# Optimization experiments

Measured on AMD Instinct MI355X. Metric: run time of the kernel, lower is better.

## Reference

```python
import jax, jax.numpy as jnp
import numpy as np

B, I, E, X, T, W = 32768, 512, 8, 128, 2, 64


def setup_inputs() -> dict:
    key = jax.random.key(0)
    ks = jax.random.split(key, 6)
    sc = lambda k, shape, s: (jax.random.normal(k, shape, jnp.float32) * s)
    return {
        "x": jax.random.normal(ks[0], (B, I), jnp.float32),
        "We": sc(ks[1], (E, I, X), 0.04),       # per-expert SLP weights
        "be": jnp.zeros((E, X), jnp.float32),
        "gates": sc(ks[2], (T, I, E), 0.04),    # per-task gating matrices (no softmax in original)
        "tW1": sc(ks[3], (T, X, W), 0.08),      # tower MLP layer 1
        "tb1": jnp.zeros((T, W), jnp.float32),
        "tW2": sc(ks[4], (T, W, 1), 0.1),       # tower MLP layer 2 (scalar head)
        "tb2": jnp.zeros((T, 1), jnp.float32),
    }


def reference(x, We, be, gates, tW1, tb1, tW2, tb2):
    # task gates: [T, B, E] (raw matmul, faithful to original: no softmax applied)
    g = jnp.einsum('bi,tie->tbe', x, gates)
    # expert SLPs (Linear + ReLU): [E, B, X]
    ex = jax.nn.relu(jnp.einsum('bi,eix->ebx', x, We) + be[:, None, :])
    # fused replacement of the nested expert_size x num_experts loop:
    # shared_info[t, b, i] = sum_j g[t,b,j] * ex[j,b,i]
    shared = jnp.einsum('tbe,ebx->tbx', g, ex)
    # tower MLPs: Linear -> ReLU -> Linear(1)
    h = jax.nn.relu(jnp.einsum('tbx,txw->tbw', shared, tW1) + tb1[:, None, :])
    out = jnp.einsum('tbw,two->tbo', h, tW2) + tb2[:, None, :]
    return out  # [T, B, 1], row t = task t's output
```

## Files before the change

kernel.cpp:

```cpp
#include <hip/hip_runtime.h>
#include <cstdint>
#include <cstddef>

#define NB 32768
#define KI 512
#define NE 8
#define NX 128
#define NT 2
#define NWD 64
#define BM 128
#define THREADS 512
#define SMEM_BYTES 163840
#define W2_BYTES (NE * KI * NX * 2)

typedef __attribute__((ext_vector_type(8))) short bf16x8;
typedef __attribute__((ext_vector_type(4))) float f32x4;

__device__ __forceinline__ unsigned short f2bf(float f) {
  union { float f; unsigned u; } v; v.f = f;
  return (unsigned short)((v.u + 0x7fffu + ((v.u >> 16) & 1u)) >> 16);
}

#define AS1(p) ((const __attribute__((address_space(1))) void*)(uintptr_t)(p))
#define AS3(p) ((__attribute__((address_space(3))) void*)(uintptr_t)(p))

__global__ __launch_bounds__(256) void repack_we_kernel(const float* __restrict__ We,
                                                        unsigned short* __restrict__ W2) {
  int tid = blockIdx.x * 256 + threadIdx.x;
  int col  = tid & (NX - 1);
  int kblk = (tid >> 7) & 63;
  int e    = tid >> 13;
  const float* src = We + ((size_t)e * KI + (size_t)kblk * 8) * NX + col;
  bf16x8 v;
#pragma unroll
  for (int j = 0; j < 8; ++j) v[j] = (short)f2bf(src[(size_t)j * NX]);
  *(bf16x8*)(W2 + (size_t)tid * 8) = v;
}

template <bool USE_WS>
__global__ __launch_bounds__(THREADS, 2)
void moe_fused_kernel(const float* __restrict__ x, const float* __restrict__ We,
                      const float* __restrict__ be, const float* __restrict__ gates,
                      const float* __restrict__ tW1, const float* __restrict__ tb1,
                      const float* __restrict__ tW2, const float* __restrict__ tb2,
                      const unsigned short* __restrict__ W2, float* __restrict__ out) {
  extern __shared__ char smem[];
  char* wbuf = smem + 131072;

  const int tid  = threadIdx.x;
  const int lane = tid & 63;
  const int wid  = tid >> 6;
  const int l15  = lane & 15;
  const int lhi  = lane >> 4;
  const int row0 = blockIdx.x * BM;

  f32x4 acc[8];
  f32x4 shacc[NT][8];
  f32x4 gacc = {0.f, 0.f, 0.f, 0.f};
#pragma unroll
  for (int t = 0; t < NT; ++t)
#pragma unroll
    for (int cf = 0; cf < 8; ++cf) shacc[t][cf] = (f32x4){0.f, 0.f, 0.f, 0.f};

  const int arow = wid * 16 + l15;
  const int asw  = (arow & 7) << 4;
  char* abase = smem + arow * 1024;

  auto stage_x = [&](int kk) {
    const int xr = tid >> 2;
    const int xs = tid & 3;
    const float* src = x + (size_t)(row0 + xr) * KI + kk * 64 + xs * 16;
    float4 a0 = ((const float4*)src)[0];
    float4 a1 = ((const float4*)src)[1];
    float4 a2 = ((const float4*)src)[2];
    float4 a3 = ((const float4*)src)[3];
    bf16x8 v0, v1;
    v0[0]=(short)f2bf(a0.x); v0[1]=(short)f2bf(a0.y); v0[2]=(short)f2bf(a0.z); v0[3]=(short)f2bf(a0.w);
    v0[4]=(short)f2bf(a1.x); v0[5]=(short)f2bf(a1.y); v0[6]=(short)f2bf(a1.z); v0[7]=(short)f2bf(a1.w);
    v1[0]=(short)f2bf(a2.x); v1[1]=(short)f2bf(a2.y); v1[2]=(short)f2bf(a2.z); v1[3]=(short)f2bf(a2.w);
    v1[4]=(short)f2bf(a3.x); v1[5]=(short)f2bf(a3.y); v1[6]=(short)f2bf(a3.z); v1[7]=(short)f2bf(a3.w);
    const int sw = (xr & 7) << 4;
    const int kb = kk * 128 + xs * 32;
    *(bf16x8*)(smem + xr * 1024 + ((kb) ^ sw)) = v0;
    *(bf16x8*)(smem + xr * 1024 + ((kb + 16) ^ sw)) = v1;
  };

  auto stage_w = [&](int e, int kk, int b) {
    if constexpr (USE_WS) {
      const char* gbase = (const char*)W2 + ((size_t)(e * 64 + kk * 8) * NX) * 16;
      char* lbase = wbuf + b * 16384 + wid * 1024;
      __builtin_amdgcn_global_load_lds(AS1(gbase + (wid * 64 + lane) * 16), AS3(lbase), 16, 0, 0);
      __builtin_amdgcn_global_load_lds(AS1(gbase + 8192 + (wid * 64 + lane) * 16), AS3(lbase + 8192), 16, 0, 0);
    } else {
      const int col = tid & 127;
      const int kb0 = tid >> 7;
#pragma unroll
      for (int h = 0; h < 2; ++h) {
        const int kblk = kb0 + h * 4;
        const float* src = We + ((size_t)e * KI + (size_t)(kk * 64 + kblk * 8)) * NX + col;
        bf16x8 v;
#pragma unroll
        for (int j = 0; j < 8; ++j) v[j] = (short)f2bf(src[(size_t)j * NX]);
        *(bf16x8*)(wbuf + b * 16384 + (kblk * NX + col) * 16) = v;
      }
    }
  };

  auto compute_chunk = [&](int kk, int b) {
#pragma unroll
    for (int ks = 0; ks < 2; ++ks) {
      bf16x8 a = *(const bf16x8*)(abase + ((kk * 128 + ks * 64 + lhi * 16) ^ asw));
      const char* bbase = wbuf + b * 16384 + ((ks * 4 + lhi) * NX + l15) * 16;
#pragma unroll
      for (int cf = 0; cf < 8; ++cf) {
        bf16x8 bfr = *(const bf16x8*)(bbase + cf * 256);
        acc[cf] = __builtin_amdgcn_mfma_f32_16x16x32_bf16(a, bfr, acc[cf], 0, 0, 0);
      }
    }
  };

  auto compute_g = [&]() {
    const int ct = l15 >> 3;
    const int ce = l15 & 7;
#pragma unroll
    for (int ks = 0; ks < 16; ++ks) {
      bf16x8 a = *(const bf16x8*)(abase + ((ks * 64 + lhi * 16) ^ asw));
      const float* gsrc = gates + (size_t)ct * (KI * NE) + (size_t)(ks * 32 + lhi * 8) * NE + ce;
      bf16x8 bv;
#pragma unroll
      for (int j = 0; j < 8; ++j) bv[j] = (short)f2bf(gsrc[j * NE]);
      gacc = __builtin_amdgcn_mfma_f32_16x16x32_bf16(a, bv, gacc, 0, 0, 0);
    }
  };

  auto epilogue = [&](int e) {
    float gv[NT][4];
#pragma unroll
    for (int t = 0; t < NT; ++t)
#pragma unroll
      for (int r = 0; r < 4; ++r)
        gv[t][r] = __shfl(gacc[r], (lane & 48) | (t * 8 + e), 64);
#pragma unroll
    for (int cf = 0; cf < 8; ++cf) {
      const float bev = be[e * NX + cf * 16 + l15];
#pragma unroll
      for (int r = 0; r < 4; ++r) {
        float ex = acc[cf][r] + bev;
        ex = fmaxf(ex, 0.f);
        shacc[0][cf][r] += gv[0][r] * ex;
        shacc[1][cf][r] += gv[1][r] * ex;
      }
    }
  };

  for (int e = 0; e < NE; ++e) {
#pragma unroll
    for (int cf = 0; cf < 8; ++cf) acc[cf] = (f32x4){0.f, 0.f, 0.f, 0.f};
    if (e == 0) stage_x(0);
    stage_w(e, 0, 0);
    __syncthreads();
    for (int kk = 0; kk < 8; ++kk) {
      if (kk < 7) {
        if (e == 0) stage_x(kk + 1);
        stage_w(e, kk + 1, (kk + 1) & 1);
      }
      compute_chunk(kk, kk & 1);
      __syncthreads();
    }
    if (e == 0) compute_g();
    epilogue(e);
  }

#pragma unroll
  for (int t = 0; t < NT; ++t)
#pragma unroll
    for (int cf = 0; cf < 8; ++cf)
#pragma unroll
      for (int r = 0; r < 4; ++r) {
        const int rr = wid * 16 + lhi * 4 + r;
        const int cc = cf * 16 + l15;
        *(unsigned short*)(smem + t * 32768 + rr * 256 + ((cc * 2) ^ ((rr & 7) << 4))) =
            f2bf(shacc[t][cf][r]);
      }
  __syncthreads();

#pragma unroll
  for (int t = 0; t < NT; ++t) {
    f32x4 hacc[4];
#pragma unroll
    for (int cf = 0; cf < 4; ++cf) hacc[cf] = (f32x4){0.f, 0.f, 0.f, 0.f};
    const int trow = wid * 16 + l15;
    const char* tbase = smem + t * 32768 + trow * 256;
    const int tsw = (trow & 7) << 4;
#pragma unroll
    for (int ks = 0; ks < 4; ++ks) {
      bf16x8 a = *(const bf16x8*)(tbase + ((ks * 64 + lhi * 16) ^ tsw));
#pragma unroll
      for (int cf = 0; cf < 4; ++cf) {
        const int col = cf * 16 + l15;
        const float* wsrc = tW1 + (size_t)t * (NX * NWD) + (size_t)(ks * 32 + lhi * 8) * NWD + col;
        bf16x8 bv;
#pragma unroll
        for (int j = 0; j < 8; ++j) bv[j] = (short)f2bf(wsrc[j * NWD]);
        hacc[cf] = __builtin_amdgcn_mfma_f32_16x16x32_bf16(a, bv, hacc[cf], 0, 0, 0);
      }
    }
    float p[4] = {0.f, 0.f, 0.f, 0.f};
#pragma unroll
    for (int cf = 0; cf < 4; ++cf) {
      const int col = cf * 16 + l15;
      const float b1 = tb1[t * NWD + col];
      const float w2 = tW2[t * NWD + col];
#pragma unroll
      for (int r = 0; r < 4; ++r) {
        float h = fmaxf(hacc[cf][r] + b1, 0.f);
        p[r] += h * w2;
      }
    }
#pragma unroll
    for (int r = 0; r < 4; ++r) {
      p[r] += __shfl_xor(p[r], 1, 64);
      p[r] += __shfl_xor(p[r], 2, 64);
      p[r] += __shfl_xor(p[r], 4, 64);
      p[r] += __shfl_xor(p[r], 8, 64);
    }
    if (l15 == 0) {
      const float b2 = tb2[t];
#pragma unroll
      for (int r = 0; r < 4; ++r)
        out[(size_t)t * NB + row0 + wid * 16 + lhi * 4 + r] = p[r] + b2;
    }
  }
}

extern "C" void kernel_launch(void* const* d_in, const int* in_sizes, int n_in,
                              void* d_out, int out_size, void* d_ws, size_t ws_size,
                              hipStream_t stream) {
  const float* x     = (const float*)d_in[0];
  const float* We    = (const float*)d_in[1];
  const float* be    = (const float*)d_in[2];
  const float* gates = (const float*)d_in[3];
  const float* tW1   = (const float*)d_in[4];
  const float* tb1   = (const float*)d_in[5];
  const float* tW2   = (const float*)d_in[6];
  const float* tb2   = (const float*)d_in[7];
  float* out = (float*)d_out;

  const bool use_ws = (d_ws != nullptr) && (ws_size >= (size_t)W2_BYTES);
  const int nblk = NB / BM;

  if (use_ws) {
    unsigned short* W2 = (unsigned short*)d_ws;
    hipFuncSetAttribute(reinterpret_cast<const void*>(moe_fused_kernel<true>),
                        hipFuncAttributeMaxDynamicSharedMemorySize, SMEM_BYTES);
    repack_we_kernel<<<(NE * KI * NX / 8) / 256, 256, 0, stream>>>(We, W2);
    moe_fused_kernel<true><<<nblk, THREADS, SMEM_BYTES, stream>>>(
        x, We, be, gates, tW1, tb1, tW2, tb2, W2, out);
  } else {
    hipFuncSetAttribute(reinterpret_cast<const void*>(moe_fused_kernel<false>),
                        hipFuncAttributeMaxDynamicSharedMemorySize, SMEM_BYTES);
    moe_fused_kernel<false><<<nblk, THREADS, SMEM_BYTES, stream>>>(
        x, We, be, gates, tW1, tb1, tW2, tb2, nullptr, out);
  }
}
```

Measured before the change: 66.69 us.

## Load expert weights directly from global into registers, shrink tile to 64 rows

```diff
diff --git a/kernel.cpp b/kernel.cpp
--- a/kernel.cpp
+++ b/kernel.cpp
@@ -8,10 +8,16 @@
 #define NX 128
 #define NT 2
 #define NWD 64
-#define BM 128
-#define THREADS 512
-#define SMEM_BYTES 163840
-#define W2_BYTES (NE * KI * NX * 2)
+#define BM 64
+#define THREADS 256
+#define SMEM_BYTES 65536
+
+#define W2_ELEMS (NE * KI * NX)
+#define G2_OFF   W2_ELEMS
+#define G2_ELEMS (64 * 16 * 8)
+#define T2_OFF   (G2_OFF + G2_ELEMS)
+#define T2_ELEMS (NT * 16 * 64 * 8)
+#define WS_NEED  ((size_t)(W2_ELEMS + G2_ELEMS + T2_ELEMS) * 2)
 
 typedef __attribute__((ext_vector_type(8))) short bf16x8;
 typedef __attribute__((ext_vector_type(4))) float f32x4;
@@ -21,11 +27,8 @@
   return (unsigned short)((v.u + 0x7fffu + ((v.u >> 16) & 1u)) >> 16);
 }
 
-#define AS1(p) ((const __attribute__((address_space(1))) void*)(uintptr_t)(p))
-#define AS3(p) ((__attribute__((address_space(3))) void*)(uintptr_t)(p))
-
 __global__ __launch_bounds__(256) void repack_we_kernel(const float* __restrict__ We,
-                                                        unsigned short* __restrict__ W2) {
+                                                        unsigned short* __restrict__ ws) {
   int tid = blockIdx.x * 256 + threadIdx.x;
   int col  = tid & (NX - 1);
   int kblk = (tid >> 7) & 63;
@@ -34,7 +37,34 @@
   bf16x8 v;
 #pragma unroll
   for (int j = 0; j < 8; ++j) v[j] = (short)f2bf(src[(size_t)j * NX]);
-  *(bf16x8*)(W2 + (size_t)tid * 8) = v;
+  *(bf16x8*)(ws + (size_t)tid * 8) = v;
+}
+
+__global__ __launch_bounds__(256) void repack_aux_kernel(const float* __restrict__ gates,
+                                                         const float* __restrict__ tW1,
+                                                         unsigned short* __restrict__ ws) {
+  int tid = threadIdx.x;
+#pragma unroll
+  for (int i = 0; i < 4; ++i) {
+    int f = i * 256 + tid;
+    int kb = f >> 4, col = f & 15;
+    int t = col >> 3, e = col & 7;
+    const float* src = gates + (size_t)t * (KI * NE) + (size_t)(kb * 8) * NE + e;
+    bf16x8 v;
+#pragma unroll
+    for (int j = 0; j < 8; ++j) v[j] = (short)f2bf(src[(size_t)j * NE]);
+    *(bf16x8*)(ws + G2_OFF + (size_t)f * 8) = v;
+  }
+#pragma unroll
+  for (int i = 0; i < 8; ++i) {
+    int f = i * 256 + tid;
+    int t = f >> 10, kb = (f >> 6) & 15, col = f & 63;
+    const float* src = tW1 + (size_t)t * (NX * NWD) + (size_t)(kb * 8) * NWD + col;
+    bf16x8 v;
+#pragma unroll
+    for (int j = 0; j < 8; ++j) v[j] = (short)f2bf(src[(size_t)j * NWD]);
+    *(bf16x8*)(ws + T2_OFF + (size_t)f * 8) = v;
+  }
 }
 
 template <bool USE_WS>
@@ -43,179 +73,198 @@
                       const float* __restrict__ be, const float* __restrict__ gates,
                       const float* __restrict__ tW1, const float* __restrict__ tb1,
                       const float* __restrict__ tW2, const float* __restrict__ tb2,
-                      const unsigned short* __restrict__ W2, float* __restrict__ out) {
+                      const unsigned short* __restrict__ ws, float* __restrict__ out) {
   extern __shared__ char smem[];
-  char* wbuf = smem + 131072;
-
   const int tid  = threadIdx.x;
   const int lane = tid & 63;
   const int wid  = tid >> 6;
   const int l15  = lane & 15;
   const int lhi  = lane >> 4;
+  const int wr   = wid >> 1;
+  const int wc   = wid & 1;
   const int row0 = blockIdx.x * BM;
 
-  f32x4 acc[8];
-  f32x4 shacc[NT][8];
-  f32x4 gacc = {0.f, 0.f, 0.f, 0.f};
+  {
+    const float4* xs4 = (const float4*)(x + (size_t)row0 * KI);
+#pragma unroll
+    for (int c = 0; c < 16; ++c) {
+      int i = c * 256 + tid;
+      float4 a0 = xs4[(size_t)i * 2];
+      float4 a1 = xs4[(size_t)i * 2 + 1];
+      bf16x8 v;
+      v[0] = (short)f2bf(a0.x); v[1] = (short)f2bf(a0.y);
+      v[2] = (short)f2bf(a0.z); v[3] = (short)f2bf(a0.w);
+      v[4] = (short)f2bf(a1.x); v[5] = (short)f2bf(a1.y);
+      v[6] = (short)f2bf(a1.z); v[7] = (short)f2bf(a1.w);
+      int row = i >> 6;
+      int kb  = (i & 63) * 16;
+      *(bf16x8*)(smem + row * 1024 + (kb ^ ((row & 7) << 4))) = v;
+    }
+  }
+  __syncthreads();
+
+  auto loadBfrag = [&](int e, int kblk, int cf) -> bf16x8 {
+    if constexpr (USE_WS) {
+      return *(const bf16x8*)(ws + ((size_t)(e * 64 + kblk) * NX + wc * 64 + cf * 16 + l15) * 8);
+    } else {
+      const float* src = We + ((size_t)e * KI + (size_t)kblk * 8) * NX + wc * 64 + cf * 16 + l15;
+      bf16x8 v;
+#pragma unroll
+      for (int j = 0; j < 8; ++j) v[j] = (short)f2bf(src[(size_t)j * NX]);
+      return v;
+    }
+  };
+  auto loadGfrag = [&](int kb) -> bf16x8 {
+    if constexpr (USE_WS) {
+      return *(const bf16x8*)(ws + G2_OFF + ((size_t)kb * 16 + l15) * 8);
+    } else {
+      int t = l15 >> 3, e = l15 & 7;
+      const float* src = gates + (size_t)t * (KI * NE) + (size_t)(kb * 8) * NE + e;
+      bf16x8 v;
+#pragma unroll
+      for (int j = 0; j < 8; ++j) v[j] = (short)f2bf(src[(size_t)j * NE]);
+      return v;
+    }
+  };
+  auto loadTfrag = [&](int t, int kb, int cf) -> bf16x8 {
+    if constexpr (USE_WS) {
+      return *(const bf16x8*)(ws + T2_OFF + ((size_t)(t * 16 + kb) * 64 + cf * 16 + l15) * 8);
+    } else {
+      const float* src = tW1 + (size_t)t * (NX * NWD) + (size_t)(kb * 8) * NWD + cf * 16 + l15;
+      bf16x8 v;
+#pragma unroll
+      for (int j = 0; j < 8; ++j) v[j] = (short)f2bf(src[(size_t)j * NWD]);
+      return v;
+    }
+  };
+
+  const int arow = wr * 32 + l15;
+  char* ab0 = smem + arow * 1024;
+  char* ab1 = smem + (arow + 16) * 1024;
+  const int asw = (arow & 7) << 4;
+  auto loadA = [&](int kk, int ks, int rf) -> bf16x8 {
+    int byte = (kk * 128 + ks * 64 + lhi * 16) ^ asw;
+    return *(const bf16x8*)((rf ? ab1 : ab0) + byte);
+  };
+
+  f32x4 acc[2][4];
+  f32x4 shacc[NT][2][4];
+  f32x4 gacc[2];
 #pragma unroll
   for (int t = 0; t < NT; ++t)
 #pragma unroll
-    for (int cf = 0; cf < 8; ++cf) shacc[t][cf] = (f32x4){0.f, 0.f, 0.f, 0.f};
-
-  const int arow = wid * 16 + l15;
-  const int asw  = (arow & 7) << 4;
-  char* abase = smem + arow * 1024;
-
-  auto stage_x = [&](int kk) {
-    const int xr = tid >> 2;
-    const int xs = tid & 3;
-    const float* src = x + (size_t)(row0 + xr) * KI + kk * 64 + xs * 16;
-    float4 a0 = ((const float4*)src)[0];
-    float4 a1 = ((const float4*)src)[1];
-    float4 a2 = ((const float4*)src)[2];
-    float4 a3 = ((const float4*)src)[3];
-    bf16x8 v0, v1;
-    v0[0]=(short)f2bf(a0.x); v0[1]=(short)f2bf(a0.y); v0[2]=(short)f2bf(a0.z); v0[3]=(short)f2bf(a0.w);
-    v0[4]=(short)f2bf(a1.x); v0[5]=(short)f2bf(a1.y); v0[6]=(short)f2bf(a1.z); v0[7]=(short)f2bf(a1.w);
-    v1[0]=(short)f2bf(a2.x); v1[1]=(short)f2bf(a2.y); v1[2]=(short)f2bf(a2.z); v1[3]=(short)f2bf(a2.w);
-    v1[4]=(short)f2bf(a3.x); v1[5]=(short)f2bf(a3.y); v1[6]=(short)f2bf(a3.z); v1[7]=(short)f2bf(a3.w);
-    const int sw = (xr & 7) << 4;
-    const int kb = kk * 128 + xs * 32;
-    *(bf16x8*)(smem + xr * 1024 + ((kb) ^ sw)) = v0;
-    *(bf16x8*)(smem + xr * 1024 + ((kb + 16) ^ sw)) = v1;
-  };
-
-  auto stage_w = [&](int e, int kk, int b) {
-    if constexpr (USE_WS) {
-      const char* gbase = (const char*)W2 + ((size_t)(e * 64 + kk * 8) * NX) * 16;
-      char* lbase = wbuf + b * 16384 + wid * 1024;
-      __builtin_amdgcn_global_load_lds(AS1(gbase + (wid * 64 + lane) * 16), AS3(lbase), 16, 0, 0);
-      __builtin_amdgcn_global_load_lds(AS1(gbase + 8192 + (wid * 64 + lane) * 16), AS3(lbase + 8192), 16, 0, 0);
-    } else {
-      const int col = tid & 127;
-      const int kb0 = tid >> 7;
-#pragma unroll
-      for (int h = 0; h < 2; ++h) {
-        const int kblk = kb0 + h * 4;
-        const float* src = We + ((size_t)e * KI + (size_t)(kk * 64 + kblk * 8)) * NX + col;
-        bf16x8 v;
-#pragma unroll
-        for (int j = 0; j < 8; ++j) v[j] = (short)f2bf(src[(size_t)j * NX]);
-        *(bf16x8*)(wbuf + b * 16384 + (kblk * NX + col) * 16) = v;
+    for (int rf = 0; rf < 2; ++rf)
+#pragma unroll
+      for (int cf = 0; cf < 4; ++cf) shacc[t][rf][cf] = (f32x4){0.f, 0.f, 0.f, 0.f};
+  gacc[0] = (f32x4){0.f, 0.f, 0.f, 0.f};
+  gacc[1] = (f32x4){0.f, 0.f, 0.f, 0.f};
+
+  bf16x8 b0[8], b1[8];
+  auto loadBset = [&](bf16x8(&dst)[8], int e, int kk) {
+#pragma unroll
+    for (int ks = 0; ks < 2; ++ks)
+#pragma unroll
+      for (int cf = 0; cf < 4; ++cf)
+        dst[ks * 4 + cf] = loadBfrag(e, kk * 8 + ks * 4 + lhi, cf);
+  };
+
+  loadBset(b0, 0, 0);
+#pragma unroll
+  for (int gks = 0; gks < 16; ++gks) {
+    bf16x8 gb = loadGfrag(gks * 4 + lhi);
+    gacc[0] = __builtin_amdgcn_mfma_f32_16x16x32_bf16(loadA(gks >> 1, gks & 1, 0), gb, gacc[0], 0, 0, 0);
+    gacc[1] = __builtin_amdgcn_mfma_f32_16x16x32_bf16(loadA(gks >> 1, gks & 1, 1), gb, gacc[1], 0, 0, 0);
+  }
+
+  auto chunk = [&](bf16x8(&cur)[8], bf16x8(&nxt)[8], int e, int kk) {
+    const int ne_ = (kk == 7) ? ((e + 1) & 7) : e;
+    const int nk  = (kk == 7) ? 0 : kk + 1;
+    loadBset(nxt, ne_, nk);
+#pragma unroll
+    for (int ks = 0; ks < 2; ++ks) {
+      bf16x8 a0v = loadA(kk, ks, 0);
+      bf16x8 a1v = loadA(kk, ks, 1);
+#pragma unroll
+      for (int cf = 0; cf < 4; ++cf) {
+        acc[0][cf] = __builtin_amdgcn_mfma_f32_16x16x32_bf16(a0v, cur[ks * 4 + cf], acc[0][cf], 0, 0, 0);
+        acc[1][cf] = __builtin_amdgcn_mfma_f32_16x16x32_bf16(a1v, cur[ks * 4 + cf], acc[1][cf], 0, 0, 0);
       }
     }
   };
 
-  auto compute_chunk = [&](int kk, int b) {
-#pragma unroll
-    for (int ks = 0; ks < 2; ++ks) {
-      bf16x8 a = *(const bf16x8*)(abase + ((kk * 128 + ks * 64 + lhi * 16) ^ asw));
-      const char* bbase = wbuf + b * 16384 + ((ks * 4 + lhi) * NX + l15) * 16;
-#pragma unroll
-      for (int cf = 0; cf < 8; ++cf) {
-        bf16x8 bfr = *(const bf16x8*)(bbase + cf * 256);
-        acc[cf] = __builtin_amdgcn_mfma_f32_16x16x32_bf16(a, bfr, acc[cf], 0, 0, 0);
+  auto epilogue = [&](int e) {
+#pragma unroll
+    for (int rf = 0; rf < 2; ++rf) {
+      float gv0[4], gv1[4];
+#pragma unroll
+      for (int r = 0; r < 4; ++r) {
+        gv0[r] = __shfl(gacc[rf][r], (lane & 48) | e, 64);
+        gv1[r] = __shfl(gacc[rf][r], (lane & 48) | (8 + e), 64);
       }
-    }
-  };
-
-  auto compute_g = [&]() {
-    const int ct = l15 >> 3;
-    const int ce = l15 & 7;
-#pragma unroll
-    for (int ks = 0; ks < 16; ++ks) {
-      bf16x8 a = *(const bf16x8*)(abase + ((ks * 64 + lhi * 16) ^ asw));
-      const float* gsrc = gates + (size_t)ct * (KI * NE) + (size_t)(ks * 32 + lhi * 8) * NE + ce;
-      bf16x8 bv;
-#pragma unroll
-      for (int j = 0; j < 8; ++j) bv[j] = (short)f2bf(gsrc[j * NE]);
-      gacc = __builtin_amdgcn_mfma_f32_16x16x32_bf16(a, bv, gacc, 0, 0, 0);
-    }
-  };
-
-  auto epilogue = [&](int e) {
-    float gv[NT][4];
-#pragma unroll
-    for (int t = 0; t < NT; ++t)
-#pragma unroll
-      for (int r = 0; r < 4; ++r)
-        gv[t][r] = __shfl(gacc[r], (lane & 48) | (t * 8 + e), 64);
-#pragma unroll
-    for (int cf = 0; cf < 8; ++cf) {
-      const float bev = be[e * NX + cf * 16 + l15];
-#pragma unroll
-      for (int r = 0; r < 4; ++r) {
-        float ex = acc[cf][r] + bev;
-        ex = fmaxf(ex, 0.f);
-        shacc[0][cf][r] += gv[0][r] * ex;
-        shacc[1][cf][r] += gv[1][r] * ex;
+#pragma unroll
+      for (int cf = 0; cf < 4; ++cf) {
+        const float bev = be[e * NX + wc * 64 + cf * 16 + l15];
+#pragma unroll
+        for (int r = 0; r < 4; ++r) {
+          float ex = fmaxf(acc[rf][cf][r] + bev, 0.f);
+          shacc[0][rf][cf][r] += gv0[r] * ex;
+          shacc[1][rf][cf][r] += gv1[r] * ex;
+        }
       }
     }
   };
 
   for (int e = 0; e < NE; ++e) {
 #pragma unroll
-    for (int cf = 0; cf < 8; ++cf) acc[cf] = (f32x4){0.f, 0.f, 0.f, 0.f};
-    if (e == 0) stage_x(0);
-    stage_w(e, 0, 0);
-    __syncthreads();
-    for (int kk = 0; kk < 8; ++kk) {
-      if (kk < 7) {
-        if (e == 0) stage_x(kk + 1);
-        stage_w(e, kk + 1, (kk + 1) & 1);
-      }
-      compute_chunk(kk, kk & 1);
-      __syncthreads();
-    }
-    if (e == 0) compute_g();
+    for (int rf = 0; rf < 2; ++rf)
+#pragma unroll
+      for (int cf = 0; cf < 4; ++cf) acc[rf][cf] = (f32x4){0.f, 0.f, 0.f, 0.f};
+    chunk(b0, b1, e, 0); chunk(b1, b0, e, 1);
+    chunk(b0, b1, e, 2); chunk(b1, b0, e, 3);
+    chunk(b0, b1, e, 4); chunk(b1, b0, e, 5);
+    chunk(b0, b1, e, 6); chunk(b1, b0, e, 7);
     epilogue(e);
   }
 
+  __syncthreads();
 #pragma unroll
   for (int t = 0; t < NT; ++t)
 #pragma unroll
-    for (int cf = 0; cf < 8; ++cf)
-#pragma unroll
-      for (int r = 0; r < 4; ++r) {
-        const int rr = wid * 16 + lhi * 4 + r;
-        const int cc = cf * 16 + l15;
-        *(unsigned short*)(smem + t * 32768 + rr * 256 + ((cc * 2) ^ ((rr & 7) << 4))) =
-            f2bf(shacc[t][cf][r]);
-      }
+    for (int rf = 0; rf < 2; ++rf)
+#pragma unroll
+      for (int cf = 0; cf < 4; ++cf)
+#pragma unroll
+        for (int r = 0; r < 4; ++r) {
+          int row = wr * 32 + rf * 16 + lhi * 4 + r;
+          int col = wc * 64 + cf * 16 + l15;
+          *(unsigned short*)(smem + t * 16384 + row * 256 + ((col * 2) ^ ((row & 7) << 4))) =
+              f2bf(shacc[t][rf][cf][r]);
+        }
   __syncthreads();
 
+  const int trow = wid * 16 + l15;
+  const char* tbase = smem + trow * 256;
+  const int tsw = (trow & 7) << 4;
 #pragma unroll
   for (int t = 0; t < NT; ++t) {
     f32x4 hacc[4];
 #pragma unroll
     for (int cf = 0; cf < 4; ++cf) hacc[cf] = (f32x4){0.f, 0.f, 0.f, 0.f};
-    const int trow = wid * 16 + l15;
-    const char* tbase = smem + t * 32768 + trow * 256;
-    const int tsw = (trow & 7) << 4;
 #pragma unroll
     for (int ks = 0; ks < 4; ++ks) {
-      bf16x8 a = *(const bf16x8*)(tbase + ((ks * 64 + lhi * 16) ^ tsw));
-#pragma unroll
-      for (int cf = 0; cf < 4; ++cf) {
-        const int col = cf * 16 + l15;
-        const float* wsrc = tW1 + (size_t)t * (NX * NWD) + (size_t)(ks * 32 + lhi * 8) * NWD + col;
-        bf16x8 bv;
-#pragma unroll
-        for (int j = 0; j < 8; ++j) bv[j] = (short)f2bf(wsrc[j * NWD]);
-        hacc[cf] = __builtin_amdgcn_mfma_f32_16x16x32_bf16(a, bv, hacc[cf], 0, 0, 0);
-      }
+      bf16x8 a = *(const bf16x8*)(tbase + t * 16384 + ((ks * 64 + lhi * 16) ^ tsw));
+#pragma unroll
+      for (int cf = 0; cf < 4; ++cf)
+        hacc[cf] = __builtin_amdgcn_mfma_f32_16x16x32_bf16(a, loadTfrag(t, ks * 4 + lhi, cf), hacc[cf], 0, 0, 0);
     }
     float p[4] = {0.f, 0.f, 0.f, 0.f};
 #pragma unroll
     for (int cf = 0; cf < 4; ++cf) {
-      const int col = cf * 16 + l15;
-      const float b1 = tb1[t * NWD + col];
-      const float w2 = tW2[t * NWD + col];
-#pragma unroll
-      for (int r = 0; r < 4; ++r) {
-        float h = fmaxf(hacc[cf][r] + b1, 0.f);
-        p[r] += h * w2;
-      }
+      int col = cf * 16 + l15;
+      const float b1v = tb1[t * NWD + col];
+      const float w2v = tW2[t * NWD + col];
+#pragma unroll
+      for (int r = 0; r < 4; ++r) p[r] += fmaxf(hacc[cf][r] + b1v, 0.f) * w2v;
     }
 #pragma unroll
     for (int r = 0; r < 4; ++r) {
@@ -226,9 +275,9 @@
     }
     if (l15 == 0) {
       const float b2 = tb2[t];
-#pragma unroll
-      for (int r = 0; r < 4; ++r)
-        out[(size_t)t * NB + row0 + wid * 16 + lhi * 4 + r] = p[r] + b2;
+      float4 o;
+      o.x = p[0] + b2; o.y = p[1] + b2; o.z = p[2] + b2; o.w = p[3] + b2;
+      *(float4*)(out + (size_t)t * NB + row0 + wid * 16 + lhi * 4) = o;
     }
   }
 }
@@ -246,16 +295,17 @@
   const float* tb2   = (const float*)d_in[7];
   float* out = (float*)d_out;
 
-  const bool use_ws = (d_ws != nullptr) && (ws_size >= (size_t)W2_BYTES);
+  const bool use_ws = (d_ws != nullptr) && (ws_size >= WS_NEED);
   const int nblk = NB / BM;
 
   if (use_ws) {
-    unsigned short* W2 = (unsigned short*)d_ws;
+    unsigned short* ws = (unsigned short*)d_ws;
     hipFuncSetAttribute(reinterpret_cast<const void*>(moe_fused_kernel<true>),
                         hipFuncAttributeMaxDynamicSharedMemorySize, SMEM_BYTES);
-    repack_we_kernel<<<(NE * KI * NX / 8) / 256, 256, 0, stream>>>(We, W2);
+    repack_we_kernel<<<(W2_ELEMS / 8) / 256, 256, 0, stream>>>(We, ws);
+    repack_aux_kernel<<<1, 256, 0, stream>>>(gates, tW1, ws);
     moe_fused_kernel<true><<<nblk, THREADS, SMEM_BYTES, stream>>>(
-        x, We, be, gates, tW1, tb1, tW2, tb2, W2, out);
+        x, We, be, gates, tW1, tb1, tW2, tb2, ws, out);
   } else {
     hipFuncSetAttribute(reinterpret_cast<const void*>(moe_fused_kernel<false>),
                         hipFuncAttributeMaxDynamicSharedMemorySize, SMEM_BYTES);
```

After: 166.8 us. 2.5x slower.
